# Performance work log

Hardware: AMD Instinct MI355X
Metric: run time of the kernel (lower is better)

Reference implementation:

```python
import jax, jax.numpy as jnp
import numpy as np

N = 50000      # nodes
E = 800000     # edges (before self loops)
F_IN = 128     # input feature dim
H = 4          # attention heads
C = 64         # per-head channels (hidden_dim = out_channels = 64)
HC = H * C     # 256, concat output width of each GATv2Conv
G = 32         # number of graphs in the batch
NEG_SLOPE_ATT = 0.2   # GATv2 internal LeakyReLU
NEG_SLOPE_ACT = 0.01  # encoder nn.LeakyReLU() default


def _glorot(key, shape, fan_in):
    return jax.random.normal(key, shape, jnp.float32) * (1.0 / np.sqrt(fan_in))


def setup_inputs() -> dict:
    key = jax.random.key(0)
    ks = jax.random.split(key, 32)
    inp = {}
    inp["x"] = jax.random.normal(ks[0], (N, F_IN), jnp.float32)
    inp["edge_index"] = jax.random.randint(ks[1], (2, E), 0, N, jnp.int32)
    inp["batch"] = jnp.sort(jax.random.randint(ks[2], (N,), 0, G, jnp.int32))
    i = 3
    for li, fin in ((1, F_IN), (2, HC), (3, HC)):
        inp[f"Wl{li}"] = _glorot(ks[i], (HC, fin), fin); i += 1
        inp[f"bl{li}"] = jnp.zeros((HC,), jnp.float32)
        inp[f"Wr{li}"] = _glorot(ks[i], (HC, fin), fin); i += 1
        inp[f"br{li}"] = jnp.zeros((HC,), jnp.float32)
        inp[f"att{li}"] = _glorot(ks[i], (H, C), C); i += 1
        inp[f"bo{li}"] = jnp.zeros((HC,), jnp.float32)
    return inp


def _gatv2_layer(x, src, dst, Wl, bl, Wr, br, att, bo):
    n = x.shape[0]
    xl = (x @ Wl.T + bl).reshape(n, H, C)  # source transform
    xr = (x @ Wr.T + br).reshape(n, H, C)  # target transform
    # per-edge attention logits: a^T LeakyReLU(xl[j] + xr[i])
    e = jax.nn.leaky_relu(xl[src] + xr[dst], negative_slope=NEG_SLOPE_ATT)  # [E', H, C]
    score = jnp.einsum('ehc,hc->eh', e, att)                                # [E', H]
    # segment softmax over incoming edges of each destination node
    m = jax.ops.segment_max(score, dst, num_segments=n)
    p = jnp.exp(score - m[dst])
    s = jax.ops.segment_sum(p, dst, num_segments=n)
    alpha = p / s[dst]
    out = jax.ops.segment_sum(alpha[:, :, None] * xl[src], dst, num_segments=n)
    return out.reshape(n, HC) + bo


def reference(x, edge_index, batch,
              Wl1, bl1, Wr1, br1, att1, bo1,
              Wl2, bl2, Wr2, br2, att2, bo2,
              Wl3, bl3, Wr3, br3, att3, bo3):
    loop = jnp.arange(N, dtype=edge_index.dtype)
    src = jnp.concatenate([edge_index[0], loop])  # add self loops (PyG default)
    dst = jnp.concatenate([edge_index[1], loop])
    h = _gatv2_layer(x, src, dst, Wl1, bl1, Wr1, br1, att1, bo1)
    h = jax.nn.leaky_relu(h, negative_slope=NEG_SLOPE_ACT)
    h = _gatv2_layer(h, src, dst, Wl2, bl2, Wr2, br2, att2, bo2)
    h = jax.nn.leaky_relu(h, negative_slope=NEG_SLOPE_ACT)
    h = _gatv2_layer(h, src, dst, Wl3, bl3, Wr3, br3, att3, bo3)
    # global mean pool over graphs
    sums = jax.ops.segment_sum(h, batch, num_segments=G)
    cnt = jax.ops.segment_sum(jnp.ones((N,), h.dtype), batch, num_segments=G)
    return sums / jnp.maximum(cnt, 1.0)[:, None]
```

## Files before the change

kernel.cpp:

```cpp
#include <hip/hip_runtime.h>

#define HEADS 4
#define CH 64
#define HC 256
#define NGRAPH 32
#define NEG_ATT 0.2f
#define NEG_ACT 0.01f

typedef __attribute__((ext_vector_type(8))) short bf16x8;
typedef __attribute__((ext_vector_type(4))) float f32x4;

__device__ __forceinline__ void split2(float a, float b, unsigned& hi, unsigned& lo) {
  unsigned ua = __float_as_uint(a), ub = __float_as_uint(b);
  float la = a - __uint_as_float(ua & 0xFFFF0000u);
  float lb = b - __uint_as_float(ub & 0xFFFF0000u);
  hi = __builtin_amdgcn_perm(ub, ua, 0x07060302u);
  lo = __builtin_amdgcn_perm(__float_as_uint(lb), __float_as_uint(la), 0x07060302u);
}

__device__ __forceinline__ unsigned rtn_bf16(float f) {
  unsigned u = __float_as_uint(f);
  return (u + 0x7FFFu + ((u >> 16) & 1u)) >> 16;
}

__global__ __launch_bounds__(256) void convert_x(
    const float* __restrict__ X, unsigned short* __restrict__ xhi,
    unsigned short* __restrict__ xlo, int total4) {
  int g = blockIdx.x * 256 + threadIdx.x;
  if (g >= total4) return;
  float4 v = *(const float4*)&X[(size_t)g * 4];
  uint2 h2, l2;
  split2(v.x, v.y, h2.x, l2.x);
  split2(v.z, v.w, h2.y, l2.y);
  *(uint2*)&xhi[(size_t)g * 4] = h2;
  *(uint2*)&xlo[(size_t)g * 4] = l2;
}

__global__ __launch_bounds__(256) void convert_w(
    const float* __restrict__ Wl, const float* __restrict__ Wr,
    unsigned short* __restrict__ whi, unsigned short* __restrict__ wlo, int K) {
  int g = blockIdx.x * 256 + threadIdx.x;
  int e4 = g * 4;
  int half = 256 * K;
  const float* src = (e4 < half) ? &Wl[e4] : &Wr[e4 - half];
  float4 v = *(const float4*)src;
  uint2 h2, l2;
  split2(v.x, v.y, h2.x, l2.x);
  split2(v.z, v.w, h2.y, l2.y);
  *(uint2*)&whi[(size_t)e4] = h2;
  *(uint2*)&wlo[(size_t)e4] = l2;
}

__global__ __launch_bounds__(256) void gemm_fused(
    const unsigned short* __restrict__ xhi, const unsigned short* __restrict__ xlo,
    const unsigned short* __restrict__ whi, const unsigned short* __restrict__ wlo,
    const float* __restrict__ bl, const float* __restrict__ br,
    unsigned short* __restrict__ Y1, float* __restrict__ Y2, int N, int K) {
  __shared__ unsigned short Ahi[128][32];
  __shared__ unsigned short Alo[128][32];
  __shared__ unsigned short Bhi[128][32];
  __shared__ unsigned short Blo[128][32];

  const int tid = threadIdx.x;
  const int wave = tid >> 6;
  const int lane = tid & 63;
  const int quad = lane >> 4;
  const int l16 = lane & 15;
  const int wr = (wave >> 1) * 64;
  const int wc = (wave & 1) * 64;
  const int col0 = blockIdx.x * 128;
  const int row0 = blockIdx.y * 128;

  f32x4 acc[4][4];
#pragma unroll
  for (int i = 0; i < 4; i++)
#pragma unroll
    for (int j = 0; j < 4; j++) acc[i][j] = (f32x4){0.f, 0.f, 0.f, 0.f};

  const int r_s = tid >> 2;
  const int c_s = (tid & 3) * 8;

  for (int k0 = 0; k0 < K; k0 += 32) {
#pragma unroll
    for (int it = 0; it < 2; it++) {
      int r = r_s + it * 64;
      int gr = row0 + r;
      if (gr >= N) gr = N - 1;
      size_t ga = (size_t)gr * K + k0 + c_s;
      *(uint4*)&Ahi[r][c_s] = *(const uint4*)&xhi[ga];
      *(uint4*)&Alo[r][c_s] = *(const uint4*)&xlo[ga];
      size_t gb = (size_t)(col0 + r) * K + k0 + c_s;
      *(uint4*)&Bhi[r][c_s] = *(const uint4*)&whi[gb];
      *(uint4*)&Blo[r][c_s] = *(const uint4*)&wlo[gb];
    }
    __syncthreads();

    bf16x8 ahi[4], alo[4], bhi[4], blo[4];
#pragma unroll
    for (int i = 0; i < 4; i++) {
      ahi[i] = *(const bf16x8*)&Ahi[wr + i * 16 + l16][quad * 8];
      alo[i] = *(const bf16x8*)&Alo[wr + i * 16 + l16][quad * 8];
      bhi[i] = *(const bf16x8*)&Bhi[wc + i * 16 + l16][quad * 8];
      blo[i] = *(const bf16x8*)&Blo[wc + i * 16 + l16][quad * 8];
    }
#pragma unroll
    for (int i = 0; i < 4; i++)
#pragma unroll
      for (int j = 0; j < 4; j++) {
        acc[i][j] = __builtin_amdgcn_mfma_f32_16x16x32_bf16(ahi[i], bhi[j], acc[i][j], 0, 0, 0);
        acc[i][j] = __builtin_amdgcn_mfma_f32_16x16x32_bf16(ahi[i], blo[j], acc[i][j], 0, 0, 0);
        acc[i][j] = __builtin_amdgcn_mfma_f32_16x16x32_bf16(alo[i], bhi[j], acc[i][j], 0, 0, 0);
      }
    __syncthreads();
  }

#pragma unroll
  for (int j = 0; j < 4; j++) {
    int colg = col0 + wc + j * 16 + l16;
    if (colg < HC) {
      float bv = bl[colg];
#pragma unroll
      for (int i = 0; i < 4; i++)
#pragma unroll
        for (int r = 0; r < 4; r++) {
          int row = row0 + wr + i * 16 + quad * 4 + r;
          if (row < N)
            Y1[(size_t)row * HC + colg] = (unsigned short)rtn_bf16(acc[i][j][r] + bv);
        }
    } else {
      int cc = colg - HC;
      float bv = br[cc];
#pragma unroll
      for (int i = 0; i < 4; i++)
#pragma unroll
        for (int r = 0; r < 4; r++) {
          int row = row0 + wr + i * 16 + quad * 4 + r;
          if (row < N) Y2[(size_t)row * HC + cc] = acc[i][j][r] + bv;
        }
    }
  }
}

__global__ __launch_bounds__(256) void hist_dst(
    const int* __restrict__ edst, int* __restrict__ counts, int E) {
  int e = blockIdx.x * 256 + threadIdx.x;
  if (e < E) atomicAdd(&counts[edst[e]], 1);
}

__global__ __launch_bounds__(256) void scan_blocks(
    const int* __restrict__ counts, int* __restrict__ row_start,
    int* __restrict__ bsum, int N) {
  __shared__ int tmp[256];
  int t = threadIdx.x;
  int base = blockIdx.x * 1024 + t * 4;
  int v0 = (base     < N) ? counts[base]     + 1 : 0;
  int v1 = (base + 1 < N) ? counts[base + 1] + 1 : 0;
  int v2 = (base + 2 < N) ? counts[base + 2] + 1 : 0;
  int v3 = (base + 3 < N) ? counts[base + 3] + 1 : 0;
  int c1 = v0 + v1, c2 = c1 + v2, tot = c2 + v3;
  tmp[t] = tot;
  __syncthreads();
  for (int off = 1; off < 256; off <<= 1) {
    int add = (t >= off) ? tmp[t - off] : 0;
    __syncthreads();
    tmp[t] += add;
    __syncthreads();
  }
  int excl = tmp[t] - tot;
  if (base     < N) row_start[base + 1] = excl + v0;
  if (base + 1 < N) row_start[base + 2] = excl + c1;
  if (base + 2 < N) row_start[base + 3] = excl + c2;
  if (base + 3 < N) row_start[base + 4] = excl + tot;
  if (t == 255) bsum[blockIdx.x] = tmp[255];
  if (blockIdx.x == 0 && t == 0) row_start[0] = 0;
}

__global__ void scan_tops(int* __restrict__ bsum, int nb) {
  int lane = threadIdx.x;
  int v = (lane < nb) ? bsum[lane] : 0;
  for (int off = 1; off < 64; off <<= 1) {
    int u = __shfl_up(v, off);
    if (lane >= off) v += u;
  }
  if (lane < nb) bsum[lane] = v;
}

__global__ __launch_bounds__(256) void scan_add(
    int* __restrict__ row_start, const int* __restrict__ bsum, int N) {
  int off = bsum[blockIdx.x];
  int i = (blockIdx.x + 1) * 1024 + threadIdx.x * 4;
#pragma unroll
  for (int k = 0; k < 4; k++)
    if (i + k < N) row_start[i + k + 1] += off;
}

__global__ __launch_bounds__(256) void csr_init(
    const int* __restrict__ row_start, int* __restrict__ fill_pos,
    int* __restrict__ csr_src, int N) {
  int i = blockIdx.x * 256 + threadIdx.x;
  if (i < N) {
    int p = row_start[i];
    csr_src[p] = i;
    fill_pos[i] = p + 1;
  }
}

__global__ __launch_bounds__(256) void csr_scatter(
    const int* __restrict__ esrc, const int* __restrict__ edst,
    int* __restrict__ fill_pos, int* __restrict__ csr_src, int E) {
  int e = blockIdx.x * 256 + threadIdx.x;
  if (e < E) {
    int p = atomicAdd(&fill_pos[edst[e]], 1);
    csr_src[p] = esrc[e];
  }
}

__device__ __forceinline__ float4 unpack_bf16x4(uint2 q) {
  float4 r;
  r.x = __uint_as_float(q.x << 16);
  r.y = __uint_as_float(q.x & 0xFFFF0000u);
  r.z = __uint_as_float(q.y << 16);
  r.w = __uint_as_float(q.y & 0xFFFF0000u);
  return r;
}

__device__ __forceinline__ float edge_dot(const float4 lv, const float4 rv, const float4 a) {
  float t, d = 0.f;
  t = lv.x + rv.x; t = t > 0.f ? t : NEG_ATT * t; d = fmaf(t, a.x, d);
  t = lv.y + rv.y; t = t > 0.f ? t : NEG_ATT * t; d = fmaf(t, a.y, d);
  t = lv.z + rv.z; t = t > 0.f ? t : NEG_ATT * t; d = fmaf(t, a.z, d);
  t = lv.w + rv.w; t = t > 0.f ? t : NEG_ATT * t; d = fmaf(t, a.w, d);
  d += __shfl_xor(d, 1);
  d += __shfl_xor(d, 2);
  d += __shfl_xor(d, 4);
  d += __shfl_xor(d, 8);
  return d;
}

__global__ __launch_bounds__(256) void gat_fused(
    const unsigned short* __restrict__ xl, const float* __restrict__ xr,
    const int* __restrict__ row_start, const int* __restrict__ csr_src,
    const float* __restrict__ att, const float* __restrict__ bo,
    float* __restrict__ outf, unsigned short* __restrict__ ohi,
    unsigned short* __restrict__ olo, int N, int split_out) {
  int dst = (blockIdx.x * 256 + threadIdx.x) >> 6;
  int lane = threadIdx.x & 63;
  if (dst >= N) return;
  int h = lane >> 4;
  int off = h * CH + (lane & 15) * 4;
  const float4 a = *(const float4*)&att[off];
  const float4 rv = *(const float4*)&xr[(size_t)dst * HC + off];
  float4 o = {0.f, 0.f, 0.f, 0.f};
  float m = -__builtin_inff();
  float s = 0.f;
  int p = row_start[dst];
  int end = row_start[dst + 1];
  for (; p + 4 <= end; p += 4) {
    int s0 = csr_src[p + 0], s1 = csr_src[p + 1];
    int s2 = csr_src[p + 2], s3 = csr_src[p + 3];
    const float4 lv0 = unpack_bf16x4(*(const uint2*)&xl[(size_t)s0 * HC + off]);
    const float4 lv1 = unpack_bf16x4(*(const uint2*)&xl[(size_t)s1 * HC + off]);
    const float4 lv2 = unpack_bf16x4(*(const uint2*)&xl[(size_t)s2 * HC + off]);
    const float4 lv3 = unpack_bf16x4(*(const uint2*)&xl[(size_t)s3 * HC + off]);
    float d0 = edge_dot(lv0, rv, a);
    float d1 = edge_dot(lv1, rv, a);
    float d2 = edge_dot(lv2, rv, a);
    float d3 = edge_dot(lv3, rv, a);
    float newm = fmaxf(fmaxf(fmaxf(d0, d1), fmaxf(d2, d3)), m);
    float sc = __expf(m - newm);
    float e0 = __expf(d0 - newm), e1 = __expf(d1 - newm);
    float e2 = __expf(d2 - newm), e3 = __expf(d3 - newm);
    s = fmaf(s, sc, (e0 + e1) + (e2 + e3));
    o.x = fmaf(o.x, sc, fmaf(e0, lv0.x, fmaf(e1, lv1.x, fmaf(e2, lv2.x, e3 * lv3.x))));
    o.y = fmaf(o.y, sc, fmaf(e0, lv0.y, fmaf(e1, lv1.y, fmaf(e2, lv2.y, e3 * lv3.y))));
    o.z = fmaf(o.z, sc, fmaf(e0, lv0.z, fmaf(e1, lv1.z, fmaf(e2, lv2.z, e3 * lv3.z))));
    o.w = fmaf(o.w, sc, fmaf(e0, lv0.w, fmaf(e1, lv1.w, fmaf(e2, lv2.w, e3 * lv3.w))));
    m = newm;
  }
  for (; p < end; p++) {
    int src = csr_src[p];
    const float4 lv = unpack_bf16x4(*(const uint2*)&xl[(size_t)src * HC + off]);
    float d = edge_dot(lv, rv, a);
    float newm = fmaxf(m, d);
    float sc = __expf(m - newm);
    float pe = __expf(d - newm);
    s = fmaf(s, sc, pe);
    o.x = fmaf(o.x, sc, pe * lv.x);
    o.y = fmaf(o.y, sc, pe * lv.y);
    o.z = fmaf(o.z, sc, pe * lv.z);
    o.w = fmaf(o.w, sc, pe * lv.w);
    m = newm;
  }
  float inv = 1.f / s;
  const float4 b4 = *(const float4*)&bo[off];
  float4 res;
  res.x = fmaf(o.x, inv, b4.x);
  res.y = fmaf(o.y, inv, b4.y);
  res.z = fmaf(o.z, inv, b4.z);
  res.w = fmaf(o.w, inv, b4.w);
  if (split_out) {
    res.x = res.x > 0.f ? res.x : NEG_ACT * res.x;
    res.y = res.y > 0.f ? res.y : NEG_ACT * res.y;
    res.z = res.z > 0.f ? res.z : NEG_ACT * res.z;
    res.w = res.w > 0.f ? res.w : NEG_ACT * res.w;
    uint2 h2, l2;
    split2(res.x, res.y, h2.x, l2.x);
    split2(res.z, res.w, h2.y, l2.y);
    *(uint2*)&ohi[(size_t)dst * HC + off] = h2;
    *(uint2*)&olo[(size_t)dst * HC + off] = l2;
  } else {
    *(float4*)&outf[(size_t)dst * HC + off] = res;
  }
}

__global__ __launch_bounds__(256) void pool_partial(
    const float* __restrict__ h, const int* __restrict__ batch,
    float* __restrict__ out, int* __restrict__ cnt, int N) {
  __shared__ float part[NGRAPH][HC];
  __shared__ int bsh[256];
  __shared__ int cpart[NGRAPH];
  int j = threadIdx.x;
#pragma unroll
  for (int g = 0; g < NGRAPH; g++) part[g][j] = 0.f;
  if (j < NGRAPH) cpart[j] = 0;
  int n0 = blockIdx.x * 256;
  int nend = min(n0 + 256, N);
  int nj = n0 + j;
  bsh[j] = (nj < N) ? batch[nj] : 0;
  __syncthreads();
  if (nj < nend) atomicAdd(&cpart[bsh[j]], 1);
  for (int n = n0; n < nend; n++) {
    int g = bsh[n - n0];
    part[g][j] += h[(size_t)n * HC + j];
  }
  __syncthreads();
#pragma unroll
  for (int g = 0; g < NGRAPH; g++) {
    float v = part[g][j];
    if (v != 0.f) atomicAdd(&out[g * HC + j], v);
  }
  if (j < NGRAPH && cpart[j] > 0) atomicAdd(&cnt[j], cpart[j]);
}

__global__ __launch_bounds__(256) void pool_final(
    float* __restrict__ out, const int* __restrict__ cnt) {
  int g = blockIdx.x;
  int j = threadIdx.x;
  float c = (float)max(cnt[g], 1);
  out[g * HC + j] /= c;
}

extern "C" void kernel_launch(void* const* d_in, const int* in_sizes, int n_in,
                              void* d_out, int out_size, void* d_ws, size_t ws_size,
                              hipStream_t stream) {
  const float* x = (const float*)d_in[0];
  const int* ei = (const int*)d_in[1];
  const int* batch = (const int*)d_in[2];
  const int N = in_sizes[2];
  const int E = in_sizes[1] / 2;
  const int Etot = E + N;

  const float* Wl[3] = {(const float*)d_in[3], (const float*)d_in[9], (const float*)d_in[15]};
  const float* bl[3] = {(const float*)d_in[4], (const float*)d_in[10], (const float*)d_in[16]};
  const float* Wr[3] = {(const float*)d_in[5], (const float*)d_in[11], (const float*)d_in[17]};
  const float* br[3] = {(const float*)d_in[6], (const float*)d_in[12], (const float*)d_in[18]};
  const float* att[3] = {(const float*)d_in[7], (const float*)d_in[13], (const float*)d_in[19]};
  const float* bo[3] = {(const float*)d_in[8], (const float*)d_in[14], (const float*)d_in[20]};

  float* B0 = (float*)d_ws;
  float* B1 = B0 + (size_t)N * HC;
  float* B2 = B1 + (size_t)N * HC;
  unsigned short* w1hi = (unsigned short*)(B2 + (size_t)N * HC);
  unsigned short* w1lo = w1hi + 512 * 128;
  unsigned short* w2hi = w1lo + 512 * 128;
  unsigned short* w2lo = w2hi + 512 * 256;
  unsigned short* w3hi = w2lo + 512 * 256;
  unsigned short* w3lo = w3hi + 512 * 256;
  int* counts = (int*)(w3lo + 512 * 256);
  int* row_start = counts + N;
  int* bsum = row_start + N + 1;
  int* fill_pos = bsum + 64;
  int* csr_src = fill_pos + N;
  int* cnt = csr_src + Etot;

  unsigned short* xlB = (unsigned short*)B1;

  unsigned short* xhiL1 = (unsigned short*)B0;
  unsigned short* xloL1 = xhiL1 + (size_t)N * 128;
  unsigned short* xhiL = (unsigned short*)B0;
  unsigned short* xloL = xhiL + (size_t)N * HC;

  const int* esrc = ei;
  const int* edst = ei + E;

  convert_x<<<(N * 128 / 4 + 255) / 256, 256, 0, stream>>>(x, xhiL1, xloL1, N * 128 / 4);
  convert_w<<<512 * 128 / 1024, 256, 0, stream>>>(Wl[0], Wr[0], w1hi, w1lo, 128);
  convert_w<<<512 * 256 / 1024, 256, 0, stream>>>(Wl[1], Wr[1], w2hi, w2lo, 256);
  convert_w<<<512 * 256 / 1024, 256, 0, stream>>>(Wl[2], Wr[2], w3hi, w3lo, 256);

  const int nscan = (N + 1023) / 1024;
  (void)hipMemsetAsync(counts, 0, (size_t)N * sizeof(int), stream);
  hist_dst<<<(E + 255) / 256, 256, 0, stream>>>(edst, counts, E);
  scan_blocks<<<nscan, 256, 0, stream>>>(counts, row_start, bsum, N);
  scan_tops<<<1, 64, 0, stream>>>(bsum, nscan);
  scan_add<<<nscan - 1, 256, 0, stream>>>(row_start, bsum, N);
  csr_init<<<(N + 255) / 256, 256, 0, stream>>>(row_start, fill_pos, csr_src, N);
  csr_scatter<<<(E + 255) / 256, 256, 0, stream>>>(esrc, edst, fill_pos, csr_src, E);

  const dim3 ggrid(4, (N + 127) / 128);
  const int fblocks = (N * 64 + 255) / 256;

  gemm_fused<<<ggrid, 256, 0, stream>>>(xhiL1, xloL1, w1hi, w1lo, bl[0], br[0], xlB, B2, N, 128);
  gat_fused<<<fblocks, 256, 0, stream>>>(xlB, B2, row_start, csr_src, att[0], bo[0],
                                         nullptr, xhiL, xloL, N, 1);
  gemm_fused<<<ggrid, 256, 0, stream>>>(xhiL, xloL, w2hi, w2lo, bl[1], br[1], xlB, B2, N, 256);
  gat_fused<<<fblocks, 256, 0, stream>>>(xlB, B2, row_start, csr_src, att[1], bo[1],
                                         nullptr, xhiL, xloL, N, 1);
  gemm_fused<<<ggrid, 256, 0, stream>>>(xhiL, xloL, w3hi, w3lo, bl[2], br[2], xlB, B2, N, 256);
  gat_fused<<<fblocks, 256, 0, stream>>>(xlB, B2, row_start, csr_src, att[2], bo[2],
                                         B0, nullptr, nullptr, N, 0);

  (void)hipMemsetAsync(d_out, 0, NGRAPH * HC * sizeof(float), stream);
  (void)hipMemsetAsync(cnt, 0, NGRAPH * sizeof(int), stream);
  pool_partial<<<(N + 255) / 256, 256, 0, stream>>>(B0, batch, (float*)d_out, cnt, N);
  pool_final<<<NGRAPH, 256, 0, stream>>>((float*)d_out, cnt);
}
```

Measured before the change: 748.1 us.

## Pre-swizzle weights into MFMA fragments and double-buffer A tiles via direct LDS loads

```diff
diff --git a/kernel.cpp b/kernel.cpp
--- a/kernel.cpp
+++ b/kernel.cpp
@@ -9,6 +9,14 @@
 
 typedef __attribute__((ext_vector_type(8))) short bf16x8;
 typedef __attribute__((ext_vector_type(4))) float f32x4;
+
+typedef __attribute__((address_space(3))) unsigned int lds_u32;
+typedef const __attribute__((address_space(1))) unsigned int glob_u32;
+
+__device__ __forceinline__ void gl_lds16(const void* g, void* l) {
+  __builtin_amdgcn_global_load_lds((glob_u32*)(uintptr_t)g,
+                                   (lds_u32*)(unsigned int)(uintptr_t)l, 16, 0, 0);
+}
 
 __device__ __forceinline__ void split2(float a, float b, unsigned& hi, unsigned& lo) {
   unsigned ua = __float_as_uint(a), ub = __float_as_uint(b);
@@ -36,30 +44,34 @@
   *(uint2*)&xlo[(size_t)g * 4] = l2;
 }
 
-__global__ __launch_bounds__(256) void convert_w(
+__global__ __launch_bounds__(256) void convert_w_frag(
     const float* __restrict__ Wl, const float* __restrict__ Wr,
-    unsigned short* __restrict__ whi, unsigned short* __restrict__ wlo, int K) {
+    unsigned short* __restrict__ wfhi, unsigned short* __restrict__ wflo, int K) {
   int g = blockIdx.x * 256 + threadIdx.x;
-  int e4 = g * 4;
-  int half = 256 * K;
-  const float* src = (e4 < half) ? &Wl[e4] : &Wr[e4 - half];
-  float4 v = *(const float4*)src;
-  uint2 h2, l2;
-  split2(v.x, v.y, h2.x, l2.x);
-  split2(v.z, v.w, h2.y, l2.y);
-  *(uint2*)&whi[(size_t)e4] = h2;
-  *(uint2*)&wlo[(size_t)e4] = l2;
+  int lane = g & 63;
+  int ct = (g >> 6) & 31;
+  int kb = g >> 11;
+  int col = ct * 16 + (lane & 15);
+  int k = kb * 32 + (lane >> 4) * 8;
+  const float* src = (col < HC) ? &Wl[(size_t)col * K + k] : &Wr[(size_t)(col - HC) * K + k];
+  float4 v0 = *(const float4*)src;
+  float4 v1 = *(const float4*)(src + 4);
+  uint4 hq, lq;
+  split2(v0.x, v0.y, hq.x, lq.x);
+  split2(v0.z, v0.w, hq.y, lq.y);
+  split2(v1.x, v1.y, hq.z, lq.z);
+  split2(v1.z, v1.w, hq.w, lq.w);
+  *(uint4*)&wfhi[(size_t)g * 8] = hq;
+  *(uint4*)&wflo[(size_t)g * 8] = lq;
 }
 
 __global__ __launch_bounds__(256) void gemm_fused(
     const unsigned short* __restrict__ xhi, const unsigned short* __restrict__ xlo,
-    const unsigned short* __restrict__ whi, const unsigned short* __restrict__ wlo,
+    const unsigned short* __restrict__ wfhi, const unsigned short* __restrict__ wflo,
     const float* __restrict__ bl, const float* __restrict__ br,
     unsigned short* __restrict__ Y1, float* __restrict__ Y2, int N, int K) {
-  __shared__ unsigned short Ahi[128][32];
-  __shared__ unsigned short Alo[128][32];
-  __shared__ unsigned short Bhi[128][32];
-  __shared__ unsigned short Blo[128][32];
+  __shared__ unsigned short Ah[2][128][32];
+  __shared__ unsigned short Al[2][128][32];
 
   const int tid = threadIdx.x;
   const int wave = tid >> 6;
@@ -70,6 +82,14 @@
   const int wc = (wave & 1) * 64;
   const int col0 = blockIdx.x * 128;
   const int row0 = blockIdx.y * 128;
+  const int ctg0 = blockIdx.x * 8 + (wave & 1) * 4;
+  const int nkb = K >> 5;
+
+  const int c0 = tid, c1 = tid + 256;
+  const int r0g = row0 + (c0 >> 2), r1g = row0 + (c1 >> 2);
+  const int ko0 = (c0 & 3) * 8, ko1 = (c1 & 3) * 8;
+  const int gr0 = (r0g < N) ? r0g : N - 1;
+  const int gr1 = (r1g < N) ? r1g : N - 1;
 
   f32x4 acc[4][4];
 #pragma unroll
@@ -77,31 +97,40 @@
 #pragma unroll
     for (int j = 0; j < 4; j++) acc[i][j] = (f32x4){0.f, 0.f, 0.f, 0.f};
 
-  const int r_s = tid >> 2;
-  const int c_s = (tid & 3) * 8;
-
-  for (int k0 = 0; k0 < K; k0 += 32) {
-#pragma unroll
-    for (int it = 0; it < 2; it++) {
-      int r = r_s + it * 64;
-      int gr = row0 + r;
-      if (gr >= N) gr = N - 1;
-      size_t ga = (size_t)gr * K + k0 + c_s;
-      *(uint4*)&Ahi[r][c_s] = *(const uint4*)&xhi[ga];
-      *(uint4*)&Alo[r][c_s] = *(const uint4*)&xlo[ga];
-      size_t gb = (size_t)(col0 + r) * K + k0 + c_s;
-      *(uint4*)&Bhi[r][c_s] = *(const uint4*)&whi[gb];
-      *(uint4*)&Blo[r][c_s] = *(const uint4*)&wlo[gb];
+  {
+    size_t ga0 = (size_t)gr0 * K + ko0;
+    size_t ga1 = (size_t)gr1 * K + ko1;
+    gl_lds16(&xhi[ga0], &Ah[0][c0 >> 2][ko0]);
+    gl_lds16(&xlo[ga0], &Al[0][c0 >> 2][ko0]);
+    gl_lds16(&xhi[ga1], &Ah[0][c1 >> 2][ko1]);
+    gl_lds16(&xlo[ga1], &Al[0][c1 >> 2][ko1]);
+  }
+
+  int p = 0;
+  for (int kb = 0; kb < nkb; kb++) {
+    bf16x8 bhi[4], blo[4];
+#pragma unroll
+    for (int j = 0; j < 4; j++) {
+      size_t ci = ((size_t)kb * 32 + ctg0 + j) * 64 + lane;
+      bhi[j] = *(const bf16x8*)&wfhi[ci * 8];
+      blo[j] = *(const bf16x8*)&wflo[ci * 8];
     }
     __syncthreads();
-
-    bf16x8 ahi[4], alo[4], bhi[4], blo[4];
+    if (kb + 1 < nkb) {
+      int k0 = (kb + 1) * 32;
+      size_t ga0 = (size_t)gr0 * K + k0 + ko0;
+      size_t ga1 = (size_t)gr1 * K + k0 + ko1;
+      int q = p ^ 1;
+      gl_lds16(&xhi[ga0], &Ah[q][c0 >> 2][ko0]);
+      gl_lds16(&xlo[ga0], &Al[q][c0 >> 2][ko0]);
+      gl_lds16(&xhi[ga1], &Ah[q][c1 >> 2][ko1]);
+      gl_lds16(&xlo[ga1], &Al[q][c1 >> 2][ko1]);
+    }
+    bf16x8 ahi[4], alo[4];
 #pragma unroll
     for (int i = 0; i < 4; i++) {
-      ahi[i] = *(const bf16x8*)&Ahi[wr + i * 16 + l16][quad * 8];
-      alo[i] = *(const bf16x8*)&Alo[wr + i * 16 + l16][quad * 8];
-      bhi[i] = *(const bf16x8*)&Bhi[wc + i * 16 + l16][quad * 8];
-      blo[i] = *(const bf16x8*)&Blo[wc + i * 16 + l16][quad * 8];
+      ahi[i] = *(const bf16x8*)&Ah[p][wr + i * 16 + l16][quad * 8];
+      alo[i] = *(const bf16x8*)&Al[p][wr + i * 16 + l16][quad * 8];
     }
 #pragma unroll
     for (int i = 0; i < 4; i++)
@@ -111,7 +140,7 @@
         acc[i][j] = __builtin_amdgcn_mfma_f32_16x16x32_bf16(ahi[i], blo[j], acc[i][j], 0, 0, 0);
         acc[i][j] = __builtin_amdgcn_mfma_f32_16x16x32_bf16(alo[i], bhi[j], acc[i][j], 0, 0, 0);
       }
-    __syncthreads();
+    p ^= 1;
   }
 
 #pragma unroll
@@ -384,7 +413,6 @@
   int* cnt = csr_src + Etot;
 
   unsigned short* xlB = (unsigned short*)B1;
-
   unsigned short* xhiL1 = (unsigned short*)B0;
   unsigned short* xloL1 = xhiL1 + (size_t)N * 128;
   unsigned short* xhiL = (unsigned short*)B0;
@@ -394,9 +422,9 @@
   const int* edst = ei + E;
 
   convert_x<<<(N * 128 / 4 + 255) / 256, 256, 0, stream>>>(x, xhiL1, xloL1, N * 128 / 4);
-  convert_w<<<512 * 128 / 1024, 256, 0, stream>>>(Wl[0], Wr[0], w1hi, w1lo, 128);
-  convert_w<<<512 * 256 / 1024, 256, 0, stream>>>(Wl[1], Wr[1], w2hi, w2lo, 256);
-  convert_w<<<512 * 256 / 1024, 256, 0, stream>>>(Wl[2], Wr[2], w3hi, w3lo, 256);
+  convert_w_frag<<<128 * 64 / 256, 256, 0, stream>>>(Wl[0], Wr[0], w1hi, w1lo, 128);
+  convert_w_frag<<<256 * 64 / 256, 256, 0, stream>>>(Wl[1], Wr[1], w2hi, w2lo, 256);
+  convert_w_frag<<<256 * 64 / 256, 256, 0, stream>>>(Wl[2], Wr[2], w3hi, w3lo, 256);
 
   const int nscan = (N + 1023) / 1024;
   (void)hipMemsetAsync(counts, 0, (size_t)N * sizeof(int), stream);
```

Result: faster. 696.2 us (-6.9%).
